# Kernel tuning notes

Measured on AMD Instinct MI355X. Metric: run time of the kernel, lower is better.

The kernel has to match this reference:

```python
import jax, jax.numpy as jnp
import numpy as np

B, N, C, H = 4, 1024, 1024, 16
D = C // H  # head_dim = 64


def _xavier(key, shape, gain):
    fan_in, fan_out = shape[1], shape[0]
    limit = gain * np.sqrt(6.0 / (fan_in + fan_out))
    return jax.random.uniform(key, shape, jnp.float32, -limit, limit)


def setup_inputs() -> dict:
    key = jax.random.key(0)
    ks = jax.random.split(key, 12)
    g = 2.0 ** (-0.5)
    return {
        "x": jax.random.normal(ks[0], (B, N, C), jnp.float32),
        "attn_bias": jax.random.normal(ks[1], (B, H, N, N), jnp.float32),
        "attn_mask": jnp.ones((B, N), jnp.int32),
        "Wq": _xavier(ks[2], (C, C), g), "bq": jnp.zeros((C,), jnp.float32),
        "Wk": _xavier(ks[3], (C, C), g), "bk": jnp.zeros((C,), jnp.float32),
        "Wv": _xavier(ks[4], (C, C), g), "bv": jnp.zeros((C,), jnp.float32),
        "Wo": _xavier(ks[5], (C, C), 1.0), "bo": jnp.zeros((C,), jnp.float32),
    }


def reference(x, attn_bias, attn_mask, Wq, bq, Wk, bk, Wv, bv, Wo, bo):
    scale = D ** (-0.5)
    # projections; nn.Linear computes x @ W.T + b
    def proj(W, b):
        return (x @ W.T + b).reshape(B, N, H, D).transpose(0, 2, 1, 3)  # [B,H,N,D]
    q = proj(Wq, bq) * scale
    k = proj(Wk, bk)
    v = proj(Wv, bv)
    scores = jnp.einsum("bhnd,bhmd->bhnm", q, k)  # [B,H,N,N]
    scores = scores + attn_bias  # attn_bias_type == 'add'
    # 2D mask [B,N] -> [B,1,1,N]; masked_fill where mask == 0
    mask = attn_mask[:, None, None, :]
    scores = jnp.where(mask == 0, -jnp.inf, scores)
    weights = jax.nn.softmax(scores, axis=-1)  # stable (internal max subtract)
    # attn_drop is identity in eval / p=0.0
    out = jnp.einsum("bhnm,bhmd->bhnd", weights, v)
    out = out.transpose(0, 2, 1, 3).reshape(B, N, C)
    return out @ Wo.T + bo
```

## Files before the change

kernel.cpp:

```cpp
#include <hip/hip_runtime.h>
#include <hip/hip_bf16.h>

#define B_ 4
#define N_ 1024
#define C_ 1024
#define H_ 16
#define D_ 64

typedef __attribute__((ext_vector_type(8))) short bf16x8;
typedef __attribute__((ext_vector_type(4))) float f32x4;
typedef __attribute__((ext_vector_type(4))) int i32x4;

__device__ __forceinline__ void gld_lds16(const void* g, void* l) {
    __builtin_amdgcn_global_load_lds(
        (const __attribute__((address_space(1))) void*)g,
        (__attribute__((address_space(3))) void*)l, 16, 0, 0);
}

__device__ __forceinline__ unsigned cvt_pk_bf16(float lo, float hi) {
    unsigned r;
    asm("v_cvt_pk_bf16_f32 %0, %1, %2" : "=v"(r) : "v"(lo), "v"(hi));
    return r;
}

__global__ __launch_bounds__(256) void f2b_kernel(const float* __restrict__ s,
                                                  __hip_bfloat16* __restrict__ d,
                                                  int n) {
    int i = (blockIdx.x * 256 + threadIdx.x) * 4;
    if (i < n) {
        float4 v = *(const float4*)&s[i];
        d[i + 0] = __float2bfloat16(v.x);
        d[i + 1] = __float2bfloat16(v.y);
        d[i + 2] = __float2bfloat16(v.z);
        d[i + 3] = __float2bfloat16(v.w);
    }
}

__global__ __launch_bounds__(256) void f2b4_kernel(const float* __restrict__ w0,
                                                   const float* __restrict__ w1,
                                                   const float* __restrict__ w2,
                                                   const float* __restrict__ w3,
                                                   __hip_bfloat16* __restrict__ d0,
                                                   __hip_bfloat16* __restrict__ d1,
                                                   __hip_bfloat16* __restrict__ d2,
                                                   __hip_bfloat16* __restrict__ d3) {
    int sel = blockIdx.y;
    const float* s = sel == 0 ? w0 : sel == 1 ? w1 : sel == 2 ? w2 : w3;
    __hip_bfloat16* d = sel == 0 ? d0 : sel == 1 ? d1 : sel == 2 ? d2 : d3;
    int i = (blockIdx.x * 256 + threadIdx.x) * 4;
    float4 v = *(const float4*)&s[i];
    d[i + 0] = __float2bfloat16(v.x);
    d[i + 1] = __float2bfloat16(v.y);
    d[i + 2] = __float2bfloat16(v.z);
    d[i + 3] = __float2bfloat16(v.w);
}

__global__ __launch_bounds__(256) void gemm_qkv(const __hip_bfloat16* __restrict__ A,
                                                const __hip_bfloat16* __restrict__ wq,
                                                const __hip_bfloat16* __restrict__ wk,
                                                const __hip_bfloat16* __restrict__ wv,
                                                const float* __restrict__ bq,
                                                const float* __restrict__ bk,
                                                const float* __restrict__ bv,
                                                __hip_bfloat16* __restrict__ qo,
                                                __hip_bfloat16* __restrict__ ko,
                                                __hip_bfloat16* __restrict__ vto) {
    __shared__ __hip_bfloat16 Al[128 * 32];
    __shared__ __hip_bfloat16 Bl[128 * 32];
    const int sel = blockIdx.x >> 3;
    const __hip_bfloat16* Bw = sel == 0 ? wq : sel == 1 ? wk : wv;
    const float* bias = sel == 0 ? bq : sel == 1 ? bk : bv;
    const int t = threadIdx.x, w = t >> 6, l = t & 63;
    const int wr = w >> 1, wc = w & 1, lr = l & 15, lg = l >> 4;
    const int m0 = blockIdx.y * 128, n0 = (blockIdx.x & 7) * 128;
    const int K = C_;

    f32x4 acc[4][4] = {};

    for (int k0 = 0; k0 < K; k0 += 32) {
#pragma unroll
        for (int it = 0; it < 2; ++it) {
            int i = t + it * 256;
            int r = i >> 2, c8 = (i & 3) * 8;
            gld_lds16(A + (size_t)(m0 + r) * K + k0 + c8, &Al[i * 8]);
            gld_lds16(Bw + (size_t)(n0 + r) * K + k0 + c8, &Bl[i * 8]);
        }
        __syncthreads();
        bf16x8 af[4], bfr[4];
#pragma unroll
        for (int mi = 0; mi < 4; ++mi)
            af[mi] = *(const bf16x8*)&Al[(wr * 64 + mi * 16 + lr) * 32 + lg * 8];
#pragma unroll
        for (int ni = 0; ni < 4; ++ni)
            bfr[ni] = *(const bf16x8*)&Bl[(wc * 64 + ni * 16 + lr) * 32 + lg * 8];
#pragma unroll
        for (int mi = 0; mi < 4; ++mi)
#pragma unroll
            for (int ni = 0; ni < 4; ++ni)
                acc[mi][ni] = __builtin_amdgcn_mfma_f32_16x16x32_bf16(
                    af[mi], bfr[ni], acc[mi][ni], 0, 0, 0);
        __syncthreads();
    }

#pragma unroll
    for (int mi = 0; mi < 4; ++mi) {
#pragma unroll
        for (int ni = 0; ni < 4; ++ni) {
            int col = n0 + wc * 64 + ni * 16 + lr;
            float bb = bias[col];
#pragma unroll
            for (int j = 0; j < 4; ++j) {
                int row = m0 + wr * 64 + mi * 16 + lg * 4 + j;
                float v = acc[mi][ni][j] + bb;
                int bb_ = row >> 10, nn = row & 1023;
                int hh = col >> 6, dd = col & 63;
                if (sel == 0) {
                    qo[(((size_t)bb_ * H_ + hh) * N_ + nn) * D_ + dd] =
                        __float2bfloat16(v * 0.125f);
                } else if (sel == 1) {
                    ko[(((size_t)bb_ * H_ + hh) * N_ + nn) * D_ + dd] =
                        __float2bfloat16(v);
                } else {
                    vto[(((size_t)bb_ * H_ + hh) * D_ + dd) * N_ + nn] =
                        __float2bfloat16(v);
                }
            }
        }
    }
}

__global__ __launch_bounds__(256) void gemm_out(const __hip_bfloat16* __restrict__ A,
                                                const __hip_bfloat16* __restrict__ Bw,
                                                const float* __restrict__ bias,
                                                float* __restrict__ out) {
    __shared__ __hip_bfloat16 Al[128 * 32];
    __shared__ __hip_bfloat16 Bl[128 * 32];
    const int t = threadIdx.x, w = t >> 6, l = t & 63;
    const int wr = w >> 1, wc = w & 1, lr = l & 15, lg = l >> 4;
    const int m0 = blockIdx.y * 128, n0 = blockIdx.x * 128;
    const int K = C_;

    f32x4 acc[4][4] = {};

    for (int k0 = 0; k0 < K; k0 += 32) {
#pragma unroll
        for (int it = 0; it < 2; ++it) {
            int i = t + it * 256;
            int r = i >> 2, c8 = (i & 3) * 8;
            gld_lds16(A + (size_t)(m0 + r) * K + k0 + c8, &Al[i * 8]);
            gld_lds16(Bw + (size_t)(n0 + r) * K + k0 + c8, &Bl[i * 8]);
        }
        __syncthreads();
        bf16x8 af[4], bfr[4];
#pragma unroll
        for (int mi = 0; mi < 4; ++mi)
            af[mi] = *(const bf16x8*)&Al[(wr * 64 + mi * 16 + lr) * 32 + lg * 8];
#pragma unroll
        for (int ni = 0; ni < 4; ++ni)
            bfr[ni] = *(const bf16x8*)&Bl[(wc * 64 + ni * 16 + lr) * 32 + lg * 8];
#pragma unroll
        for (int mi = 0; mi < 4; ++mi)
#pragma unroll
            for (int ni = 0; ni < 4; ++ni)
                acc[mi][ni] = __builtin_amdgcn_mfma_f32_16x16x32_bf16(
                    af[mi], bfr[ni], acc[mi][ni], 0, 0, 0);
        __syncthreads();
    }

#pragma unroll
    for (int mi = 0; mi < 4; ++mi)
#pragma unroll
        for (int ni = 0; ni < 4; ++ni) {
            int col = n0 + wc * 64 + ni * 16 + lr;
            float bb = bias[col];
#pragma unroll
            for (int j = 0; j < 4; ++j) {
                int row = m0 + wr * 64 + mi * 16 + lg * 4 + j;
                out[(size_t)row * C_ + col] = acc[mi][ni][j] + bb;
            }
        }
}

#define ATTN_ITER(KT, CB, SB, BCUR, BNXT)                                          \
    {                                                                              \
        const int ktn_ = (KT) < 15 ? (KT) + 1 : 15;                                \
        gld_lds16(kg0 + (size_t)ktn_ * 4096, &Kl[SB][(w * 64) * 8]);               \
        gld_lds16(kg1 + (size_t)ktn_ * 4096, &Kl[SB][(256 + w * 64) * 8]);         \
        gld_lds16(vg0 + ktn_ * 64, &Vl[SB][(w * 64) * 8]);                         \
        gld_lds16(vg1 + ktn_ * 64, &Vl[SB][(256 + w * 64) * 8]);                   \
        _Pragma("unroll")                                                          \
        for (int nkb = 0; nkb < 4; ++nkb)                                          \
            BNXT[nkb] = *(const f32x4*)&brow[ktn_ * 64 + nkb * 16 + lg * 4];       \
        __builtin_amdgcn_sched_barrier(0);                                         \
        asm volatile("s_waitcnt vmcnt(8)" ::: "memory");                           \
        __builtin_amdgcn_sched_barrier(0);                                         \
        __builtin_amdgcn_s_barrier();                                              \
        __builtin_amdgcn_sched_barrier(0);                                         \
        const __hip_bfloat16* Kb = &Kl[CB][0];                                     \
        float s[4][4];                                                             \
        __builtin_amdgcn_s_setprio(1);                                             \
        _Pragma("unroll")                                                          \
        for (int nkb = 0; nkb < 4; ++nkb) {                                        \
            f32x4 a = {};                                                          \
            _Pragma("unroll")                                                      \
            for (int half = 0; half < 2; ++half) {                                 \
                bf16x8 kf = *(const bf16x8*)                                       \
                    &Kb[(nkb * 16 + lr) * 64 + ((half * 32 + lg * 8) ^ swz)];      \
                a = __builtin_amdgcn_mfma_f32_16x16x32_bf16(kf, qf[half], a,       \
                                                            0, 0, 0);              \
            }                                                                      \
            f32x4 pen = *(const f32x4*)&Pen[(KT) * 64 + nkb * 16 + lg * 4];        \
            _Pragma("unroll")                                                      \
            for (int j = 0; j < 4; ++j) s[nkb][j] = a[j] + BCUR[nkb][j] + pen[j];  \
        }                                                                          \
        __builtin_amdgcn_s_setprio(0);                                             \
        float tm = s[0][0];                                                        \
        _Pragma("unroll")                                                          \
        for (int nkb = 0; nkb < 4; ++nkb)                                          \
            _Pragma("unroll")                                                      \
            for (int j = 0; j < 4; ++j) tm = fmaxf(tm, s[nkb][j]);                 \
        tm = fmaxf(tm, __shfl_xor(tm, 16));                                        \
        tm = fmaxf(tm, __shfl_xor(tm, 32));                                        \
        const float mn = fmaxf(m_, tm);                                            \
        const float al = __expf(m_ - mn);                                          \
        m_ = mn;                                                                   \
        float ts = 0.f;                                                            \
        _Pragma("unroll")                                                          \
        for (int nkb = 0; nkb < 4; ++nkb)                                          \
            _Pragma("unroll")                                                      \
            for (int j = 0; j < 4; ++j) {                                          \
                float p = __expf(s[nkb][j] - mn);                                  \
                s[nkb][j] = p;                                                     \
                ts += p;                                                           \
            }                                                                      \
        ts += __shfl_xor(ts, 16);                                                  \
        ts += __shfl_xor(ts, 32);                                                  \
        l_ = l_ * al + ts;                                                         \
        unsigned pk0[4], pk1[4];                                                   \
        _Pragma("unroll")                                                          \
        for (int nkb = 0; nkb < 4; ++nkb) {                                        \
            pk0[nkb] = cvt_pk_bf16(s[nkb][0], s[nkb][1]);                          \
            pk1[nkb] = cvt_pk_bf16(s[nkb][2], s[nkb][3]);                          \
        }                                                                          \
        float alr[4];                                                              \
        _Pragma("unroll")                                                          \
        for (int j = 0; j < 4; ++j) alr[j] = __shfl(al, lg * 4 + j);               \
        _Pragma("unroll")                                                          \
        for (int db = 0; db < 4; ++db)                                             \
            _Pragma("unroll")                                                      \
            for (int j = 0; j < 4; ++j) acc[db][j] *= alr[j];                      \
        const __hip_bfloat16* Vb = &Vl[CB][0];                                     \
        __builtin_amdgcn_s_setprio(1);                                             \
        _Pragma("unroll")                                                          \
        for (int mh = 0; mh < 2; ++mh) {                                           \
            const int n0_ = 2 * mh, n1_ = 2 * mh + 1;                              \
            int e0a = __shfl((int)pk0[n0_], shi0), e0b = __shfl((int)pk0[n1_], shi0); \
            int e1a = __shfl((int)pk1[n0_], shi0), e1b = __shfl((int)pk1[n1_], shi0); \
            int e2a = __shfl((int)pk0[n0_], shi1), e2b = __shfl((int)pk0[n1_], shi1); \
            int e3a = __shfl((int)pk1[n0_], shi1), e3b = __shfl((int)pk1[n1_], shi1); \
            i32x4 pw;                                                              \
            pw[0] = lghi ? e0b : e0a;                                              \
            pw[1] = lghi ? e1b : e1a;                                              \
            pw[2] = lghi ? e2b : e2a;                                              \
            pw[3] = lghi ? e3b : e3a;                                              \
            bf16x8 paf = *(bf16x8*)&pw;                                            \
            _Pragma("unroll")                                                      \
            for (int db = 0; db < 4; ++db) {                                       \
                bf16x8 vf = *(const bf16x8*)                                       \
                    &Vb[(db * 16 + lr) * 64 + ((mh * 32 + lg * 8) ^ swz)];         \
                acc[db] = __builtin_amdgcn_mfma_f32_16x16x32_bf16(paf, vf,         \
                                                                  acc[db], 0, 0,  \
                                                                  0);              \
            }                                                                      \
        }                                                                          \
        __builtin_amdgcn_s_setprio(0);                                             \
        __builtin_amdgcn_sched_barrier(0);                                         \
        __builtin_amdgcn_s_barrier();                                              \
        __builtin_amdgcn_sched_barrier(0);                                         \
    }

__global__ __launch_bounds__(256, 4) void attn_kernel(const __hip_bfloat16* __restrict__ q,
                                                      const __hip_bfloat16* __restrict__ k,
                                                      const __hip_bfloat16* __restrict__ vt,
                                                      const float* __restrict__ bias,
                                                      const int* __restrict__ mask,
                                                      __hip_bfloat16* __restrict__ ao) {
    const int orig = blockIdx.x;
    const int wg = (orig & 7) * 128 + (orig >> 3);
    const int qt = wg & 15, h = (wg >> 4) & 15, b = wg >> 8;
    const int t = threadIdx.x, w = t >> 6, l = t & 63;
    const int lr = l & 15, lg = l >> 4;

    __shared__ __hip_bfloat16 Kl[2][64 * 64];
    __shared__ __hip_bfloat16 Vl[2][64 * 64];
    __shared__ float Pen[1024];

    const size_t bh = (size_t)b * H_ + h;
    const int qr0 = qt * 64;
    const int myrow = qr0 + w * 16 + lr;
    const int orow_base = qr0 + w * 16 + lg * 4;

    {
        int4 mi = *(const int4*)&mask[b * N_ + t * 4];
        float4 p;
        p.x = mi.x ? 0.f : -1e30f;
        p.y = mi.y ? 0.f : -1e30f;
        p.z = mi.z ? 0.f : -1e30f;
        p.w = mi.w ? 0.f : -1e30f;
        *(float4*)&Pen[t * 4] = p;
    }
    __syncthreads();

    const int c0 = t, c1 = t + 256;
    const int r0 = c0 >> 3, r1 = c1 >> 3;
    const int e0 = ((c0 & 7) * 8) ^ ((r0 & 7) << 3);
    const int e1 = ((c1 & 7) * 8) ^ ((r1 & 7) << 3);
    const __hip_bfloat16* kg0 = k + (bh * N_ + r0) * D_ + e0;
    const __hip_bfloat16* kg1 = k + (bh * N_ + r1) * D_ + e1;
    const __hip_bfloat16* vg0 = vt + (bh * D_ + r0) * N_ + e0;
    const __hip_bfloat16* vg1 = vt + (bh * D_ + r1) * N_ + e1;

    bf16x8 qf[2];
#pragma unroll
    for (int half = 0; half < 2; ++half)
        qf[half] = *(const bf16x8*)&q[(bh * N_ + myrow) * D_ + half * 32 + lg * 8];

    const float* brow = bias + ((size_t)bh * N_ + myrow) * N_;
    const int swz = (lr & 7) << 3;
    const int shi0 = ((lg & 1) << 5) + lr;
    const int shi1 = shi0 + 16;
    const bool lghi = (lg >> 1) != 0;

    f32x4 acc[4] = {};
    float m_ = -3e38f, l_ = 0.f;

    __builtin_amdgcn_sched_barrier(0);
    gld_lds16(kg0, &Kl[0][(w * 64) * 8]);
    gld_lds16(kg1, &Kl[0][(256 + w * 64) * 8]);
    gld_lds16(vg0, &Vl[0][(w * 64) * 8]);
    gld_lds16(vg1, &Vl[0][(256 + w * 64) * 8]);
    f32x4 bA[4], bB[4];
#pragma unroll
    for (int nkb = 0; nkb < 4; ++nkb)
        bA[nkb] = *(const f32x4*)&brow[nkb * 16 + lg * 4];
    __builtin_amdgcn_sched_barrier(0);

    for (int kt = 0; kt < 16; kt += 2) {
        ATTN_ITER(kt, 0, 1, bA, bB);
        ATTN_ITER(kt + 1, 1, 0, bB, bA);
    }

    float dummy = bA[0][0] + bA[1][0] + bA[2][0] + bA[3][0];
    asm volatile("" :: "v"(dummy));

    float linv[4];
#pragma unroll
    for (int j = 0; j < 4; ++j) linv[j] = 1.f / __shfl(l_, lg * 4 + j);
#pragma unroll
    for (int db = 0; db < 4; ++db)
#pragma unroll
        for (int j = 0; j < 4; ++j)
            ao[((size_t)b * N_ + orow_base + j) * C_ + h * 64 + db * 16 + lr] =
                __float2bfloat16(acc[db][j] * linv[j]);
}

extern "C" void kernel_launch(void* const* d_in, const int* in_sizes, int n_in,
                              void* d_out, int out_size, void* d_ws, size_t ws_size,
                              hipStream_t stream) {
    const float* x    = (const float*)d_in[0];
    const float* bias = (const float*)d_in[1];
    const int*   mask = (const int*)d_in[2];
    const float* Wq   = (const float*)d_in[3];
    const float* bq   = (const float*)d_in[4];
    const float* Wk   = (const float*)d_in[5];
    const float* bk   = (const float*)d_in[6];
    const float* Wv   = (const float*)d_in[7];
    const float* bv   = (const float*)d_in[8];
    const float* Wo   = (const float*)d_in[9];
    const float* bo   = (const float*)d_in[10];
    float* out = (float*)d_out;

    char* ws = (char*)d_ws;
    const size_t MB = 1u << 20;
    __hip_bfloat16* xb  = (__hip_bfloat16*)(ws + 0 * MB);
    __hip_bfloat16* wqb = (__hip_bfloat16*)(ws + 8 * MB);
    __hip_bfloat16* wkb = (__hip_bfloat16*)(ws + 10 * MB);
    __hip_bfloat16* wvb = (__hip_bfloat16*)(ws + 12 * MB);
    __hip_bfloat16* wob = (__hip_bfloat16*)(ws + 14 * MB);
    __hip_bfloat16* qb  = (__hip_bfloat16*)(ws + 16 * MB);
    __hip_bfloat16* kb  = (__hip_bfloat16*)(ws + 24 * MB);
    __hip_bfloat16* vtb = (__hip_bfloat16*)(ws + 32 * MB);
    __hip_bfloat16* aob = (__hip_bfloat16*)(ws + 40 * MB);

    f2b_kernel<<<4096, 256, 0, stream>>>(x, xb, B_ * N_ * C_);
    f2b4_kernel<<<dim3(1024, 4), 256, 0, stream>>>(Wq, Wk, Wv, Wo, wqb, wkb, wvb, wob);

    gemm_qkv<<<dim3(24, 32), 256, 0, stream>>>(xb, wqb, wkb, wvb, bq, bk, bv, qb, kb, vtb);

    attn_kernel<<<1024, 256, 0, stream>>>(qb, kb, vtb, bias, mask, aob);

    gemm_out<<<dim3(8, 32), 256, 0, stream>>>(aob, wob, bo, out);
}
```

Before: 165.5 us.

## Stage attention bias through LDS via async loads and double query tile

The attention kernel now uses 512-thread blocks covering 128 query rows, so each K/V tile in LDS is shared by twice as many waves. Bias rows are no longer loaded into registers; they go through direct global-to-LDS loads into a swizzled per-wave buffer and are read back after the QK MFMAs. The intent is to halve K/V traffic per query, free registers and make bias loads asynchronous. The risks are a larger LDS footprint (about 64KB) that may lower occupancy, and hand-tuned vmcnt/lgkmcnt waits that must match the number of loads in flight.

```diff
diff --git a/kernel.cpp b/kernel.cpp
--- a/kernel.cpp
+++ b/kernel.cpp
@@ -181,23 +181,18 @@
         }
 }
 
-#define ATTN_ITER(KT, CB, SB, BCUR, BNXT)                                          \
+#define ATTN_ITER(KT, CB, SB)                                                      \
     {                                                                              \
         const int ktn_ = (KT) < 15 ? (KT) + 1 : 15;                                \
         gld_lds16(kg0 + (size_t)ktn_ * 4096, &Kl[SB][(w * 64) * 8]);               \
-        gld_lds16(kg1 + (size_t)ktn_ * 4096, &Kl[SB][(256 + w * 64) * 8]);         \
         gld_lds16(vg0 + ktn_ * 64, &Vl[SB][(w * 64) * 8]);                         \
-        gld_lds16(vg1 + ktn_ * 64, &Vl[SB][(256 + w * 64) * 8]);                   \
-        _Pragma("unroll")                                                          \
-        for (int nkb = 0; nkb < 4; ++nkb)                                          \
-            BNXT[nkb] = *(const f32x4*)&brow[ktn_ * 64 + nkb * 16 + lg * 4];       \
-        __builtin_amdgcn_sched_barrier(0);                                         \
-        asm volatile("s_waitcnt vmcnt(8)" ::: "memory");                           \
+        __builtin_amdgcn_sched_barrier(0);                                         \
+        asm volatile("s_waitcnt vmcnt(6)" ::: "memory");                           \
         __builtin_amdgcn_sched_barrier(0);                                         \
         __builtin_amdgcn_s_barrier();                                              \
         __builtin_amdgcn_sched_barrier(0);                                         \
         const __hip_bfloat16* Kb = &Kl[CB][0];                                     \
-        float s[4][4];                                                             \
+        f32x4 a_[4];                                                               \
         __builtin_amdgcn_s_setprio(1);                                             \
         _Pragma("unroll")                                                          \
         for (int nkb = 0; nkb < 4; ++nkb) {                                        \
@@ -209,11 +204,27 @@
                 a = __builtin_amdgcn_mfma_f32_16x16x32_bf16(kf, qf[half], a,       \
                                                             0, 0, 0);              \
             }                                                                      \
-            f32x4 pen = *(const f32x4*)&Pen[(KT) * 64 + nkb * 16 + lg * 4];        \
-            _Pragma("unroll")                                                      \
-            for (int j = 0; j < 4; ++j) s[nkb][j] = a[j] + BCUR[nkb][j] + pen[j];  \
+            a_[nkb] = a;                                                           \
         }                                                                          \
         __builtin_amdgcn_s_setprio(0);                                             \
+        __builtin_amdgcn_sched_barrier(0);                                         \
+        asm volatile("s_waitcnt vmcnt(2)" ::: "memory");                           \
+        __builtin_amdgcn_sched_barrier(0);                                         \
+        float s[4][4];                                                             \
+        _Pragma("unroll")                                                          \
+        for (int nkb = 0; nkb < 4; ++nkb) {                                        \
+            f32x4 bb = *(const f32x4*)&Bb[w][lr][((nkb * 4 + lg) ^ lr) * 4];       \
+            f32x4 pen = *(const f32x4*)&Pen[(KT) * 64 + nkb * 16 + lg * 4];        \
+            _Pragma("unroll")                                                      \
+            for (int j = 0; j < 4; ++j) s[nkb][j] = a_[nkb][j] + bb[j] + pen[j];   \
+        }                                                                          \
+        __builtin_amdgcn_sched_barrier(0);                                         \
+        asm volatile("s_waitcnt lgkmcnt(0)" ::: "memory");                         \
+        __builtin_amdgcn_sched_barrier(0);                                         \
+        _Pragma("unroll")                                                          \
+        for (int i_ = 0; i_ < 4; ++i_)                                             \
+            gld_lds16(bg[i_] + ktn_ * 64, bl + i_ * 256);                          \
+        __builtin_amdgcn_sched_barrier(0);                                         \
         float tm = s[0][0];                                                        \
         _Pragma("unroll")                                                          \
         for (int nkb = 0; nkb < 4; ++nkb)                                          \
@@ -279,53 +290,56 @@
         __builtin_amdgcn_sched_barrier(0);                                         \
     }
 
-__global__ __launch_bounds__(256, 4) void attn_kernel(const __hip_bfloat16* __restrict__ q,
+__global__ __launch_bounds__(512, 4) void attn_kernel(const __hip_bfloat16* __restrict__ q,
                                                       const __hip_bfloat16* __restrict__ k,
                                                       const __hip_bfloat16* __restrict__ vt,
                                                       const float* __restrict__ bias,
                                                       const int* __restrict__ mask,
                                                       __hip_bfloat16* __restrict__ ao) {
     const int orig = blockIdx.x;
-    const int wg = (orig & 7) * 128 + (orig >> 3);
-    const int qt = wg & 15, h = (wg >> 4) & 15, b = wg >> 8;
+    const int wg = (orig & 7) * 64 + (orig >> 3);
+    const int qt = wg & 7, h = (wg >> 3) & 15, b = wg >> 7;
     const int t = threadIdx.x, w = t >> 6, l = t & 63;
     const int lr = l & 15, lg = l >> 4;
 
     __shared__ __hip_bfloat16 Kl[2][64 * 64];
     __shared__ __hip_bfloat16 Vl[2][64 * 64];
     __shared__ float Pen[1024];
+    __shared__ float Bb[8][16][64];
 
     const size_t bh = (size_t)b * H_ + h;
-    const int qr0 = qt * 64;
+    const int qr0 = qt * 128;
     const int myrow = qr0 + w * 16 + lr;
     const int orow_base = qr0 + w * 16 + lg * 4;
 
     {
-        int4 mi = *(const int4*)&mask[b * N_ + t * 4];
-        float4 p;
+        int2 mi = *(const int2*)&mask[b * N_ + t * 2];
+        float2 p;
         p.x = mi.x ? 0.f : -1e30f;
         p.y = mi.y ? 0.f : -1e30f;
-        p.z = mi.z ? 0.f : -1e30f;
-        p.w = mi.w ? 0.f : -1e30f;
-        *(float4*)&Pen[t * 4] = p;
+        *(float2*)&Pen[t * 2] = p;
     }
     __syncthreads();
 
-    const int c0 = t, c1 = t + 256;
-    const int r0 = c0 >> 3, r1 = c1 >> 3;
-    const int e0 = ((c0 & 7) * 8) ^ ((r0 & 7) << 3);
-    const int e1 = ((c1 & 7) * 8) ^ ((r1 & 7) << 3);
+    const int r0 = t >> 3;
+    const int e0 = ((t & 7) * 8) ^ ((r0 & 7) << 3);
     const __hip_bfloat16* kg0 = k + (bh * N_ + r0) * D_ + e0;
-    const __hip_bfloat16* kg1 = k + (bh * N_ + r1) * D_ + e1;
     const __hip_bfloat16* vg0 = vt + (bh * D_ + r0) * N_ + e0;
-    const __hip_bfloat16* vg1 = vt + (bh * D_ + r1) * N_ + e1;
+
+    const int rb = l >> 4, pb = l & 15;
+    const float* bg[4];
+#pragma unroll
+    for (int i = 0; i < 4; ++i) {
+        int ri = i * 4 + rb;
+        bg[i] = bias + ((size_t)bh * N_ + qr0 + w * 16 + ri) * N_ + (pb ^ ri) * 4;
+    }
+    float* bl = &Bb[w][0][0];
 
     bf16x8 qf[2];
 #pragma unroll
     for (int half = 0; half < 2; ++half)
         qf[half] = *(const bf16x8*)&q[(bh * N_ + myrow) * D_ + half * 32 + lg * 8];
 
-    const float* brow = bias + ((size_t)bh * N_ + myrow) * N_;
     const int swz = (lr & 7) << 3;
     const int shi0 = ((lg & 1) << 5) + lr;
     const int shi1 = shi0 + 16;
@@ -336,22 +350,15 @@
 
     __builtin_amdgcn_sched_barrier(0);
     gld_lds16(kg0, &Kl[0][(w * 64) * 8]);
-    gld_lds16(kg1, &Kl[0][(256 + w * 64) * 8]);
     gld_lds16(vg0, &Vl[0][(w * 64) * 8]);
-    gld_lds16(vg1, &Vl[0][(256 + w * 64) * 8]);
-    f32x4 bA[4], bB[4];
-#pragma unroll
-    for (int nkb = 0; nkb < 4; ++nkb)
-        bA[nkb] = *(const f32x4*)&brow[nkb * 16 + lg * 4];
+#pragma unroll
+    for (int i = 0; i < 4; ++i) gld_lds16(bg[i], bl + i * 256);
     __builtin_amdgcn_sched_barrier(0);
 
     for (int kt = 0; kt < 16; kt += 2) {
-        ATTN_ITER(kt, 0, 1, bA, bB);
-        ATTN_ITER(kt + 1, 1, 0, bB, bA);
-    }
-
-    float dummy = bA[0][0] + bA[1][0] + bA[2][0] + bA[3][0];
-    asm volatile("" :: "v"(dummy));
+        ATTN_ITER(kt, 0, 1);
+        ATTN_ITER(kt + 1, 1, 0);
+    }
 
     float linv[4];
 #pragma unroll
@@ -397,7 +404,7 @@
 
     gemm_qkv<<<dim3(24, 32), 256, 0, stream>>>(xb, wqb, wkb, wvb, bq, bk, bv, qb, kb, vtb);
 
-    attn_kernel<<<1024, 256, 0, stream>>>(qb, kb, vtb, bias, mask, aob);
+    attn_kernel<<<512, 512, 0, stream>>>(qb, kb, vtb, bias, mask, aob);
 
     gemm_out<<<dim3(8, 32), 256, 0, stream>>>(aob, wob, bo, out);
 }
```

After: 154.0 us. 6.9% less time.

## Enlarge attention workgroups to 256 query rows sharing K/V tiles

Applied to the files above, without the earlier changes.

The attention kernel now launches 256 workgroups of 1024 threads. Each workgroup covers 256 query rows instead of 64, so every K/V tile staged in LDS is reused by 16 waves. Loading is split by wave: half the waves load K and the other half load V. The bias prefetch moves to a two-tile-ahead scheme issued after the QK MFMAs, with the vmcnt wait adjusted to match. This cuts redundant K/V global traffic and per-block setup, but larger blocks can reduce occupancy and scheduling flexibility, and 1024-thread barriers cost more.

```diff
diff --git a/kernel.cpp b/kernel.cpp
--- a/kernel.cpp
+++ b/kernel.cpp
@@ -181,18 +181,14 @@
         }
 }
 
-#define ATTN_ITER(KT, CB, SB, BCUR, BNXT)                                          \
+#define ATTN_ITER(KT, CB, SB, BCUR)                                                \
     {                                                                              \
         const int ktn_ = (KT) < 15 ? (KT) + 1 : 15;                                \
-        gld_lds16(kg0 + (size_t)ktn_ * 4096, &Kl[SB][(w * 64) * 8]);               \
-        gld_lds16(kg1 + (size_t)ktn_ * 4096, &Kl[SB][(256 + w * 64) * 8]);         \
-        gld_lds16(vg0 + ktn_ * 64, &Vl[SB][(w * 64) * 8]);                         \
-        gld_lds16(vg1 + ktn_ * 64, &Vl[SB][(256 + w * 64) * 8]);                   \
-        _Pragma("unroll")                                                          \
-        for (int nkb = 0; nkb < 4; ++nkb)                                          \
-            BNXT[nkb] = *(const f32x4*)&brow[ktn_ * 64 + nkb * 16 + lg * 4];       \
-        __builtin_amdgcn_sched_barrier(0);                                         \
-        asm volatile("s_waitcnt vmcnt(8)" ::: "memory");                           \
+        const int ktb_ = (KT) < 14 ? (KT) + 2 : 15;                                \
+        if (w < 8) gld_lds16(kgp + (size_t)ktn_ * 4096, kld);                      \
+        else       gld_lds16(vgp + ktn_ * 64, vld);                                \
+        __builtin_amdgcn_sched_barrier(0);                                         \
+        asm volatile("s_waitcnt vmcnt(5)" ::: "memory");                           \
         __builtin_amdgcn_sched_barrier(0);                                         \
         __builtin_amdgcn_s_barrier();                                              \
         __builtin_amdgcn_sched_barrier(0);                                         \
@@ -214,6 +210,11 @@
             for (int j = 0; j < 4; ++j) s[nkb][j] = a[j] + BCUR[nkb][j] + pen[j];  \
         }                                                                          \
         __builtin_amdgcn_s_setprio(0);                                             \
+        __builtin_amdgcn_sched_barrier(0);                                         \
+        _Pragma("unroll")                                                          \
+        for (int nkb = 0; nkb < 4; ++nkb)                                          \
+            BCUR[nkb] = *(const f32x4*)&brow[ktb_ * 64 + nkb * 16 + lg * 4];       \
+        __builtin_amdgcn_sched_barrier(0);                                         \
         float tm = s[0][0];                                                        \
         _Pragma("unroll")                                                          \
         for (int nkb = 0; nkb < 4; ++nkb)                                          \
@@ -279,15 +280,15 @@
         __builtin_amdgcn_sched_barrier(0);                                         \
     }
 
-__global__ __launch_bounds__(256, 4) void attn_kernel(const __hip_bfloat16* __restrict__ q,
-                                                      const __hip_bfloat16* __restrict__ k,
-                                                      const __hip_bfloat16* __restrict__ vt,
-                                                      const float* __restrict__ bias,
-                                                      const int* __restrict__ mask,
-                                                      __hip_bfloat16* __restrict__ ao) {
+__global__ __launch_bounds__(1024, 4) void attn_kernel(const __hip_bfloat16* __restrict__ q,
+                                                       const __hip_bfloat16* __restrict__ k,
+                                                       const __hip_bfloat16* __restrict__ vt,
+                                                       const float* __restrict__ bias,
+                                                       const int* __restrict__ mask,
+                                                       __hip_bfloat16* __restrict__ ao) {
     const int orig = blockIdx.x;
-    const int wg = (orig & 7) * 128 + (orig >> 3);
-    const int qt = wg & 15, h = (wg >> 4) & 15, b = wg >> 8;
+    const int wg = (orig & 7) * 32 + (orig >> 3);
+    const int qt = wg & 3, h = (wg >> 2) & 15, b = wg >> 6;
     const int t = threadIdx.x, w = t >> 6, l = t & 63;
     const int lr = l & 15, lg = l >> 4;
 
@@ -296,29 +297,22 @@
     __shared__ float Pen[1024];
 
     const size_t bh = (size_t)b * H_ + h;
-    const int qr0 = qt * 64;
+    const int qr0 = qt * 256;
     const int myrow = qr0 + w * 16 + lr;
     const int orow_base = qr0 + w * 16 + lg * 4;
 
-    {
-        int4 mi = *(const int4*)&mask[b * N_ + t * 4];
-        float4 p;
-        p.x = mi.x ? 0.f : -1e30f;
-        p.y = mi.y ? 0.f : -1e30f;
-        p.z = mi.z ? 0.f : -1e30f;
-        p.w = mi.w ? 0.f : -1e30f;
-        *(float4*)&Pen[t * 4] = p;
-    }
+    Pen[t] = mask[b * N_ + t] ? 0.f : -1e30f;
     __syncthreads();
 
-    const int c0 = t, c1 = t + 256;
-    const int r0 = c0 >> 3, r1 = c1 >> 3;
-    const int e0 = ((c0 & 7) * 8) ^ ((r0 & 7) << 3);
-    const int e1 = ((c1 & 7) * 8) ^ ((r1 & 7) << 3);
-    const __hip_bfloat16* kg0 = k + (bh * N_ + r0) * D_ + e0;
-    const __hip_bfloat16* kg1 = k + (bh * N_ + r1) * D_ + e1;
-    const __hip_bfloat16* vg0 = vt + (bh * D_ + r0) * N_ + e0;
-    const __hip_bfloat16* vg1 = vt + (bh * D_ + r1) * N_ + e1;
+    const int u = (w < 8) ? t : (t - 512);
+    const int ru = u >> 3;
+    const int eu = ((u & 7) * 8) ^ ((ru & 7) << 3);
+    const __hip_bfloat16* kgp = k + (bh * N_ + ru) * D_ + eu;
+    const __hip_bfloat16* vgp = vt + (bh * D_ + ru) * N_ + eu;
+    __hip_bfloat16* kld0 = &Kl[0][u * 8];
+    __hip_bfloat16* vld0 = &Vl[0][u * 8];
+    __hip_bfloat16* kld1 = &Kl[1][u * 8];
+    __hip_bfloat16* vld1 = &Vl[1][u * 8];
 
     bf16x8 qf[2];
 #pragma unroll
@@ -335,22 +329,29 @@
     float m_ = -3e38f, l_ = 0.f;
 
     __builtin_amdgcn_sched_barrier(0);
-    gld_lds16(kg0, &Kl[0][(w * 64) * 8]);
-    gld_lds16(kg1, &Kl[0][(256 + w * 64) * 8]);
-    gld_lds16(vg0, &Vl[0][(w * 64) * 8]);
-    gld_lds16(vg1, &Vl[0][(256 + w * 64) * 8]);
+    if (w < 8) gld_lds16(kgp, kld0);
+    else       gld_lds16(vgp, vld0);
     f32x4 bA[4], bB[4];
 #pragma unroll
-    for (int nkb = 0; nkb < 4; ++nkb)
+    for (int nkb = 0; nkb < 4; ++nkb) {
         bA[nkb] = *(const f32x4*)&brow[nkb * 16 + lg * 4];
+        bB[nkb] = *(const f32x4*)&brow[64 + nkb * 16 + lg * 4];
+    }
     __builtin_amdgcn_sched_barrier(0);
 
     for (int kt = 0; kt < 16; kt += 2) {
-        ATTN_ITER(kt, 0, 1, bA, bB);
-        ATTN_ITER(kt + 1, 1, 0, bB, bA);
-    }
-
-    float dummy = bA[0][0] + bA[1][0] + bA[2][0] + bA[3][0];
+        {
+            __hip_bfloat16* kld = kld1; __hip_bfloat16* vld = vld1;
+            ATTN_ITER(kt, 0, 1, bA);
+        }
+        {
+            __hip_bfloat16* kld = kld0; __hip_bfloat16* vld = vld0;
+            ATTN_ITER(kt + 1, 1, 0, bB);
+        }
+    }
+
+    float dummy = bA[0][0] + bA[1][0] + bA[2][0] + bA[3][0] +
+                  bB[0][0] + bB[1][0] + bB[2][0] + bB[3][0];
     asm volatile("" :: "v"(dummy));
 
     float linv[4];
@@ -397,7 +398,7 @@
 
     gemm_qkv<<<dim3(24, 32), 256, 0, stream>>>(xb, wqb, wkb, wvb, bq, bk, bv, qb, kb, vtb);
 
-    attn_kernel<<<1024, 256, 0, stream>>>(qb, kb, vtb, bias, mask, aob);
+    attn_kernel<<<256, 1024, 0, stream>>>(qb, kb, vtb, bias, mask, aob);
 
     gemm_out<<<dim3(8, 32), 256, 0, stream>>>(aob, wob, bo, out);
 }
```

Result: faster. 158.5 us (-4.2%).
